# Optimization experiments

Measured on AMD Instinct MI355X. Metric: run time of the kernel, lower is better.

## Reference

```python
import jax, jax.numpy as jnp
import numpy as np

STRIDE = 1
PAD = 1
K = 3  # kernel size


def setup_inputs() -> dict:
    key = jax.random.key(0)
    k1, k2, k3, k4 = jax.random.split(key, 4)
    B, C, H, W, O = 4, 256, 64, 64, 256
    x = jax.random.normal(k1, (B, C, H, W), jnp.float32)
    offset = jax.random.normal(k2, (B, 2 * K * K, H, W), jnp.float32)
    mask = jax.random.uniform(k3, (B, K * K, H, W), jnp.float32)
    # kaiming-ish scale for the conv weight
    weight = jax.random.normal(k4, (O, C, K, K), jnp.float32) / np.float32(np.sqrt(C * K * K))
    return {"x": x, "offset": offset, "mask": mask, "weight": weight}


def _deform_conv2d(x, offset, mask, weight, stride=STRIDE, pad=PAD):
    """Modulated deformable conv v2 (torchvision deform_conv2d semantics)."""
    B, C, H, W = x.shape
    O, _, Kh, Kw = weight.shape
    KK = Kh * Kw
    Ho = (H + 2 * pad - Kh) // stride + 1
    Wo = (W + 2 * pad - Kw) // stride + 1

    # offset layout: [B, 2*KK, Ho, Wo], pairs are (dy, dx) per kernel tap
    off = offset.reshape(B, KK, 2, Ho, Wo)
    dy, dx = off[:, :, 0], off[:, :, 1]  # [B, KK, Ho, Wo]

    ki = (jnp.arange(KK) // Kw).astype(x.dtype)  # kernel row per tap
    kj = (jnp.arange(KK) % Kw).astype(x.dtype)   # kernel col per tap
    base_y = (jnp.arange(Ho) * stride - pad).astype(x.dtype)
    base_x = (jnp.arange(Wo) * stride - pad).astype(x.dtype)

    # sampling positions [B, KK, Ho, Wo]
    py = base_y[None, None, :, None] + ki[None, :, None, None] + dy
    px = base_x[None, None, None, :] + kj[None, :, None, None] + dx

    y0 = jnp.floor(py)
    x0 = jnp.floor(px)
    wy = py - y0  # fractional weights
    wx = px - x0
    y0i = y0.astype(jnp.int32)
    x0i = x0.astype(jnp.int32)

    x_bhwc = jnp.transpose(x, (0, 2, 3, 1))  # [B, H, W, C] for gathers
    b_idx = jnp.arange(B)[:, None, None, None]

    def gather(yi, xi):
        # zero outside the image (zero-padding bilinear sampling)
        valid = (yi >= 0) & (yi < H) & (xi >= 0) & (xi < W)
        v = x_bhwc[b_idx, jnp.clip(yi, 0, H - 1), jnp.clip(xi, 0, W - 1)]  # [B,KK,Ho,Wo,C]
        return v * valid[..., None].astype(x.dtype)

    one = jnp.asarray(1, x.dtype)
    sampled = (gather(y0i, x0i) * ((one - wy) * (one - wx))[..., None]
               + gather(y0i, x0i + 1) * ((one - wy) * wx)[..., None]
               + gather(y0i + 1, x0i) * (wy * (one - wx))[..., None]
               + gather(y0i + 1, x0i + 1) * (wy * wx)[..., None])

    sampled = sampled * mask.reshape(B, KK, Ho, Wo)[..., None]  # modulation

    # weighted accumulation == implicit GEMM over (c, kk)
    return jnp.einsum('bkhwc,ock->bohw', sampled, weight.reshape(O, C, KK))


def reference(x, offset, mask, weight):
    return _deform_conv2d(x, offset, mask, weight)
```

## Files before the change

kernel.cpp:

```cpp
#include <hip/hip_runtime.h>
#include <hip/hip_bf16.h>

#define CN 256
#define HN 64
#define WN 64
#define ON 256
#define KKN 9
#define HWN 4096
#define KDIM 2304
#define KC 288

using frag_ab = __attribute__((ext_vector_type(8))) short;
using frag_cd = __attribute__((ext_vector_type(4))) float;
using short4v = __attribute__((ext_vector_type(4))) short;
using int4v   = __attribute__((ext_vector_type(4))) int;
using float4v = __attribute__((ext_vector_type(4))) float;
using float2v = __attribute__((ext_vector_type(2))) float;
using uint2v  = __attribute__((ext_vector_type(2))) unsigned;

static __device__ inline short f2bf(float f) {
    union { float f; unsigned u; } v; v.f = f;
    unsigned r = v.u + 0x7fffu + ((v.u >> 16) & 1u);
    return (short)(r >> 16);
}

__global__ __launch_bounds__(256) void prep_kernel(const float* __restrict__ x,
                                                   const float* __restrict__ wsrc,
                                                   const float* __restrict__ offs,
                                                   const float* __restrict__ maskp,
                                                   short* __restrict__ xb16,
                                                   short* __restrict__ wtb,
                                                   int* __restrict__ descg) {
    int bidx = blockIdx.x;
    int tid  = threadIdx.x;
    if (bidx < 1024) {
        __shared__ float tile[64][65];
        int b   = bidx >> 8;
        int rem = bidx & 255;
        int c0  = (rem >> 6) * 64;
        int p0  = (rem & 63) * 64;
        int tp = tid & 63, tc = tid >> 6;
        for (int i = 0; i < 16; ++i) {
            int c = tc + i * 4;
            tile[c][tp] = x[(b * CN + c0 + c) * HWN + p0 + tp];
        }
        __syncthreads();
        int tcc = tid & 63, tpp = tid >> 6;
        for (int i = 0; i < 16; ++i) {
            int p = tpp + i * 4;
            xb16[(b * HWN + p0 + p) * CN + c0 + tcc] = f2bf(tile[tcc][p]);
        }
    } else if (bidx < 1312) {
        int chunk = (bidx - 1024) * 256 + tid;
        int ob  = chunk / (KC * 64);
        int rem = chunk - ob * (KC * 64);
        int kc  = rem >> 6;
        int row = rem & 63;
        int o   = ob * 64 + row;
        int kk  = kc >> 5;
        int oct = kc & 31;
        frag_ab v;
        #pragma unroll
        for (int e = 0; e < 8; ++e)
            v[e] = f2bf(wsrc[(o * CN + oct * 8 + e) * 9 + kk]);
        *(frag_ab*)&wtb[(size_t)chunk * 8] = v;
    } else {
        int u  = (bidx - 1312) * 256 + tid;
        int kk = u >> 14;
        int m  = u & 16383;
        int b  = m >> 12;
        int p  = m & 4095;
        int h  = p >> 6;
        int w  = p & 63;
        int ki = kk / 3, kj = kk - ki * 3;
        float dy = offs[(b * 18 + 2 * kk) * HWN + p];
        float dx = offs[(b * 18 + 2 * kk + 1) * HWN + p];
        float mv = maskp[(b * 9 + kk) * HWN + p];
        float py = (float)(h - 1 + ki) + dy;
        float px = (float)(w - 1 + kj) + dx;
        float y0f = floorf(py), x0f = floorf(px);
        float wy = py - y0f, wx = px - x0f;
        int y0 = (int)y0f, x0 = (int)x0f;
        int4v cb; float4v cw;
        #pragma unroll
        for (int cy = 0; cy < 2; ++cy)
            #pragma unroll
            for (int cx = 0; cx < 2; ++cx) {
                int yy = y0 + cy, xx = x0 + cx;
                bool valid = (yy >= 0 && yy < HN && xx >= 0 && xx < WN);
                int yc = min(max(yy, 0), HN - 1);
                int xc = min(max(xx, 0), WN - 1);
                cb[cy * 2 + cx] = ((b * HN + yc) * WN + xc) * CN;
                float wgt = (cy ? wy : 1.f - wy) * (cx ? wx : 1.f - wx) * mv;
                cw[cy * 2 + cx] = valid ? wgt : 0.f;
            }
        int* dd = descg + (size_t)u * 8;
        *(int4v*)dd       = cb;
        *(float4v*)(dd + 4) = cw;
    }
}

__global__ __launch_bounds__(256, 2) void fused_kernel(const short* __restrict__ xb16,
                                                       const short* __restrict__ wtb,
                                                       const int* __restrict__ descg,
                                                       float* __restrict__ out) {
    __shared__ struct {
        union {
            short Ab[2][8448];
            float outb[32 * 257];
        } mix;
        int desc[2304];
    } sm;
    int tid  = threadIdx.x;
    int m0   = blockIdx.x * 32;
    int b    = m0 >> 12;
    int h    = (m0 >> 6) & 63;
    int w0   = m0 & 63;
    int wv   = __builtin_amdgcn_readfirstlane(tid >> 6);
    int lane = tid & 63;
    int q    = lane >> 4, r = lane & 15;
    int wbase = 33 * (lane >> 1) * 8 + (lane & 1) * 4;
    int lane4 = lane * 4;
    int wv8   = wv * 8;

    #pragma unroll
    for (int kk = 0; kk < KKN; ++kk)
        sm.desc[kk * 256 + tid] = descg[((size_t)kk * 16384 + m0) * 8 + tid];
    __syncthreads();

    frag_cd acc[2][4];
    #pragma unroll
    for (int i = 0; i < 2; ++i)
        #pragma unroll
        for (int j = 0; j < 4; ++j)
            acc[i][j] = (frag_cd){0.f, 0.f, 0.f, 0.f};

    short4v stg[8][4];
    float4v cwc[8];

    auto prefetch = [&](int kk1) {
        #pragma unroll
        for (int i = 0; i < 8; ++i) {
            int dbase = (kk1 * 32 + wv8 + i) * 8;
            int4v cb = *(const int4v*)&sm.desc[dbase];
            cwc[i]   = *(const float4v*)&sm.desc[dbase + 4];
            #pragma unroll
            for (int c = 0; c < 4; ++c)
                stg[i][c] = *(const short4v*)&xb16[cb[c] + lane4];
        }
    };

    prefetch(0);

    for (int kk = 0; kk < KKN; ++kk) {
        short* dst = sm.mix.Ab[kk & 1];
        #pragma unroll
        for (int i = 0; i < 8; ++i) {
            float4v cw = cwc[i];
            short4v res;
            #pragma unroll
            for (int g = 0; g < 2; ++g) {
                float2v a = (float2v){0.f, 0.f};
                #pragma unroll
                for (int c = 0; c < 4; ++c) {
                    uint2v uv = __builtin_bit_cast(uint2v, stg[i][c]);
                    unsigned uu = uv[g];
                    float2v f;
                    f.x = __builtin_bit_cast(float, uu << 16);
                    f.y = __builtin_bit_cast(float, uu & 0xffff0000u);
                    a += f * cw[c];
                }
                __hip_bfloat162 p2 = __float22bfloat162_rn(make_float2(a.x, a.y));
                res[2 * g]     = *(short*)&p2.x;
                res[2 * g + 1] = *(short*)&p2.y;
            }
            *(short4v*)&dst[wbase + (wv8 + i) * 8] = res;
        }
        if (kk < 8) prefetch(kk + 1);
        __syncthreads();
        #pragma unroll
        for (int ks = 0; ks < 8; ++ks) {
            frag_ab af[2], bf[4];
            #pragma unroll
            for (int i = 0; i < 2; ++i)
                af[i] = *(const frag_ab*)
                    &dst[(33 * (ks * 4 + q) + i * 16 + r) * 8];
            #pragma unroll
            for (int j = 0; j < 4; ++j)
                bf[j] = *(const frag_ab*)
                    &wtb[(((size_t)wv * KC + kk * 32 + ks * 4 + q) * 64
                          + j * 16 + r) * 8];
            __builtin_amdgcn_s_setprio(1);
            #pragma unroll
            for (int i = 0; i < 2; ++i)
                #pragma unroll
                for (int j = 0; j < 4; ++j)
                    acc[i][j] = __builtin_amdgcn_mfma_f32_16x16x32_bf16(
                        af[i], bf[j], acc[i][j], 0, 0, 0);
            __builtin_amdgcn_s_setprio(0);
        }
    }
    __syncthreads();

    #pragma unroll
    for (int i = 0; i < 2; ++i)
        #pragma unroll
        for (int j = 0; j < 4; ++j) {
            int ml = i * 16 + q * 4;
            int ol = wv * 64 + j * 16 + r;
            sm.mix.outb[(ml + 0) * 257 + ol] = acc[i][j][0];
            sm.mix.outb[(ml + 1) * 257 + ol] = acc[i][j][1];
            sm.mix.outb[(ml + 2) * 257 + ol] = acc[i][j][2];
            sm.mix.outb[(ml + 3) * 257 + ol] = acc[i][j][3];
        }
    __syncthreads();
    {
        int ww = tid & 31;
        int og = tid >> 5;
        #pragma unroll
        for (int oo = 0; oo < 32; ++oo) {
            int o = oo * 8 + og;
            out[(((size_t)b * ON + o) * HN + h) * WN + w0 + ww] =
                sm.mix.outb[ww * 257 + o];
        }
    }
}

extern "C" void kernel_launch(void* const* d_in, const int* in_sizes, int n_in,
                              void* d_out, int out_size, void* d_ws, size_t ws_size,
                              hipStream_t stream) {
    const float* x      = (const float*)d_in[0];
    const float* offset = (const float*)d_in[1];
    const float* mask   = (const float*)d_in[2];
    const float* weight = (const float*)d_in[3];
    float* out = (float*)d_out;

    short* xb16  = (short*)d_ws;
    short* wtb   = (short*)((char*)d_ws + 8388608);
    int*   descg = (int*)((char*)d_ws + 9568256);

    hipLaunchKernelGGL(prep_kernel,  dim3(1888), dim3(256), 0, stream,
                       x, weight, offset, mask, xb16, wtb, descg);
    hipLaunchKernelGGL(fused_kernel, dim3(512),  dim3(256), 0, stream,
                       xb16, wtb, descg, out);
}
```

Measured before the change: 125.7 us.

## Compute sampling descriptors inside fused kernel and split work across 8 waves

Drops the descriptor-building stage from the prep kernel and computes the bilinear corner indices and weights directly into shared memory at the start of the fused kernel. This avoids the global write and read-back of the descriptor buffer. The fused kernel also moves to 512 threads (8 waves), and each wave now gathers 4 rows instead of 8 and computes a 32-column output slice instead of 64. That lowers register pressure per wave and should allow more waves resident, at the cost of more waves contending for the same shared-memory tile.

After: 121.3 us. 3.5% less time.

```diff
diff --git a/kernel.cpp b/kernel.cpp
--- a/kernel.cpp
+++ b/kernel.cpp
@@ -26,11 +26,8 @@
 
 __global__ __launch_bounds__(256) void prep_kernel(const float* __restrict__ x,
                                                    const float* __restrict__ wsrc,
-                                                   const float* __restrict__ offs,
-                                                   const float* __restrict__ maskp,
                                                    short* __restrict__ xb16,
-                                                   short* __restrict__ wtb,
-                                                   int* __restrict__ descg) {
+                                                   short* __restrict__ wtb) {
     int bidx = blockIdx.x;
     int tid  = threadIdx.x;
     if (bidx < 1024) {
@@ -50,7 +47,7 @@
             int p = tpp + i * 4;
             xb16[(b * HWN + p0 + p) * CN + c0 + tcc] = f2bf(tile[tcc][p]);
         }
-    } else if (bidx < 1312) {
+    } else {
         int chunk = (bidx - 1024) * 256 + tid;
         int ob  = chunk / (KC * 64);
         int rem = chunk - ob * (KC * 64);
@@ -64,45 +61,13 @@
         for (int e = 0; e < 8; ++e)
             v[e] = f2bf(wsrc[(o * CN + oct * 8 + e) * 9 + kk]);
         *(frag_ab*)&wtb[(size_t)chunk * 8] = v;
-    } else {
-        int u  = (bidx - 1312) * 256 + tid;
-        int kk = u >> 14;
-        int m  = u & 16383;
-        int b  = m >> 12;
-        int p  = m & 4095;
-        int h  = p >> 6;
-        int w  = p & 63;
-        int ki = kk / 3, kj = kk - ki * 3;
-        float dy = offs[(b * 18 + 2 * kk) * HWN + p];
-        float dx = offs[(b * 18 + 2 * kk + 1) * HWN + p];
-        float mv = maskp[(b * 9 + kk) * HWN + p];
-        float py = (float)(h - 1 + ki) + dy;
-        float px = (float)(w - 1 + kj) + dx;
-        float y0f = floorf(py), x0f = floorf(px);
-        float wy = py - y0f, wx = px - x0f;
-        int y0 = (int)y0f, x0 = (int)x0f;
-        int4v cb; float4v cw;
-        #pragma unroll
-        for (int cy = 0; cy < 2; ++cy)
-            #pragma unroll
-            for (int cx = 0; cx < 2; ++cx) {
-                int yy = y0 + cy, xx = x0 + cx;
-                bool valid = (yy >= 0 && yy < HN && xx >= 0 && xx < WN);
-                int yc = min(max(yy, 0), HN - 1);
-                int xc = min(max(xx, 0), WN - 1);
-                cb[cy * 2 + cx] = ((b * HN + yc) * WN + xc) * CN;
-                float wgt = (cy ? wy : 1.f - wy) * (cx ? wx : 1.f - wx) * mv;
-                cw[cy * 2 + cx] = valid ? wgt : 0.f;
-            }
-        int* dd = descg + (size_t)u * 8;
-        *(int4v*)dd       = cb;
-        *(float4v*)(dd + 4) = cw;
-    }
-}
-
-__global__ __launch_bounds__(256, 2) void fused_kernel(const short* __restrict__ xb16,
+    }
+}
+
+__global__ __launch_bounds__(512, 4) void fused_kernel(const short* __restrict__ xb16,
                                                        const short* __restrict__ wtb,
-                                                       const int* __restrict__ descg,
+                                                       const float* __restrict__ offs,
+                                                       const float* __restrict__ maskp,
                                                        float* __restrict__ out) {
     __shared__ struct {
         union {
@@ -121,27 +86,55 @@
     int q    = lane >> 4, r = lane & 15;
     int wbase = 33 * (lane >> 1) * 8 + (lane & 1) * 4;
     int lane4 = lane * 4;
-    int wv8   = wv * 8;
-
-    #pragma unroll
-    for (int kk = 0; kk < KKN; ++kk)
-        sm.desc[kk * 256 + tid] = descg[((size_t)kk * 16384 + m0) * 8 + tid];
+    int wv4   = wv * 4;
+
+    if (tid < 288) {
+        int kk = tid >> 5;
+        int m  = tid & 31;
+        int wc = w0 + m;
+        int p  = h * 64 + wc;
+        int ki = kk / 3, kj = kk - ki * 3;
+        float dy = offs[(b * 18 + 2 * kk) * HWN + p];
+        float dx = offs[(b * 18 + 2 * kk + 1) * HWN + p];
+        float mv = maskp[(b * 9 + kk) * HWN + p];
+        float py = (float)(h - 1 + ki) + dy;
+        float px = (float)(wc - 1 + kj) + dx;
+        float y0f = floorf(py), x0f = floorf(px);
+        float wy = py - y0f, wx = px - x0f;
+        int y0 = (int)y0f, x0 = (int)x0f;
+        int4v cb; float4v cw;
+        #pragma unroll
+        for (int cy = 0; cy < 2; ++cy)
+            #pragma unroll
+            for (int cx = 0; cx < 2; ++cx) {
+                int yy = y0 + cy, xx = x0 + cx;
+                bool valid = (yy >= 0 && yy < HN && xx >= 0 && xx < WN);
+                int yc = min(max(yy, 0), HN - 1);
+                int xc = min(max(xx, 0), WN - 1);
+                cb[cy * 2 + cx] = ((b * HN + yc) * WN + xc) * CN;
+                float wgt = (cy ? wy : 1.f - wy) * (cx ? wx : 1.f - wx) * mv;
+                cw[cy * 2 + cx] = valid ? wgt : 0.f;
+            }
+        int* dd = &sm.desc[tid * 8];
+        *(int4v*)dd       = cb;
+        *(float4v*)(dd + 4) = cw;
+    }
     __syncthreads();
 
-    frag_cd acc[2][4];
+    frag_cd acc[2][2];
     #pragma unroll
     for (int i = 0; i < 2; ++i)
         #pragma unroll
-        for (int j = 0; j < 4; ++j)
+        for (int j = 0; j < 2; ++j)
             acc[i][j] = (frag_cd){0.f, 0.f, 0.f, 0.f};
 
-    short4v stg[8][4];
-    float4v cwc[8];
+    short4v stg[4][4];
+    float4v cwc[4];
 
     auto prefetch = [&](int kk1) {
         #pragma unroll
-        for (int i = 0; i < 8; ++i) {
-            int dbase = (kk1 * 32 + wv8 + i) * 8;
+        for (int i = 0; i < 4; ++i) {
+            int dbase = (kk1 * 32 + wv4 + i) * 8;
             int4v cb = *(const int4v*)&sm.desc[dbase];
             cwc[i]   = *(const float4v*)&sm.desc[dbase + 4];
             #pragma unroll
@@ -152,10 +145,12 @@
 
     prefetch(0);
 
+    int jb = (wv & 1) * 2;
+    int ob = wv >> 1;
     for (int kk = 0; kk < KKN; ++kk) {
         short* dst = sm.mix.Ab[kk & 1];
         #pragma unroll
-        for (int i = 0; i < 8; ++i) {
+        for (int i = 0; i < 4; ++i) {
             float4v cw = cwc[i];
             short4v res;
             #pragma unroll
@@ -174,27 +169,27 @@
                 res[2 * g]     = *(short*)&p2.x;
                 res[2 * g + 1] = *(short*)&p2.y;
             }
-            *(short4v*)&dst[wbase + (wv8 + i) * 8] = res;
+            *(short4v*)&dst[wbase + (wv4 + i) * 8] = res;
         }
         if (kk < 8) prefetch(kk + 1);
         __syncthreads();
         #pragma unroll
         for (int ks = 0; ks < 8; ++ks) {
-            frag_ab af[2], bf[4];
+            frag_ab af[2], bf[2];
             #pragma unroll
             for (int i = 0; i < 2; ++i)
                 af[i] = *(const frag_ab*)
                     &dst[(33 * (ks * 4 + q) + i * 16 + r) * 8];
             #pragma unroll
-            for (int j = 0; j < 4; ++j)
+            for (int j = 0; j < 2; ++j)
                 bf[j] = *(const frag_ab*)
-                    &wtb[(((size_t)wv * KC + kk * 32 + ks * 4 + q) * 64
-                          + j * 16 + r) * 8];
+                    &wtb[(((size_t)ob * KC + kk * 32 + ks * 4 + q) * 64
+                          + (jb + j) * 16 + r) * 8];
             __builtin_amdgcn_s_setprio(1);
             #pragma unroll
             for (int i = 0; i < 2; ++i)
                 #pragma unroll
-                for (int j = 0; j < 4; ++j)
+                for (int j = 0; j < 2; ++j)
                     acc[i][j] = __builtin_amdgcn_mfma_f32_16x16x32_bf16(
                         af[i], bf[j], acc[i][j], 0, 0, 0);
             __builtin_amdgcn_s_setprio(0);
@@ -205,9 +200,9 @@
     #pragma unroll
     for (int i = 0; i < 2; ++i)
         #pragma unroll
-        for (int j = 0; j < 4; ++j) {
+        for (int j = 0; j < 2; ++j) {
             int ml = i * 16 + q * 4;
-            int ol = wv * 64 + j * 16 + r;
+            int ol = wv * 32 + j * 16 + r;
             sm.mix.outb[(ml + 0) * 257 + ol] = acc[i][j][0];
             sm.mix.outb[(ml + 1) * 257 + ol] = acc[i][j][1];
             sm.mix.outb[(ml + 2) * 257 + ol] = acc[i][j][2];
@@ -218,8 +213,8 @@
         int ww = tid & 31;
         int og = tid >> 5;
         #pragma unroll
-        for (int oo = 0; oo < 32; ++oo) {
-            int o = oo * 8 + og;
+        for (int oo = 0; oo < 16; ++oo) {
+            int o = oo * 16 + og;
             out[(((size_t)b * ON + o) * HN + h) * WN + w0 + ww] =
                 sm.mix.outb[ww * 257 + o];
         }
@@ -235,12 +230,11 @@
     const float* weight = (const float*)d_in[3];
     float* out = (float*)d_out;
 
-    short* xb16  = (short*)d_ws;
-    short* wtb   = (short*)((char*)d_ws + 8388608);
-    int*   descg = (int*)((char*)d_ws + 9568256);
-
-    hipLaunchKernelGGL(prep_kernel,  dim3(1888), dim3(256), 0, stream,
-                       x, weight, offset, mask, xb16, wtb, descg);
-    hipLaunchKernelGGL(fused_kernel, dim3(512),  dim3(256), 0, stream,
-                       xb16, wtb, descg, out);
-}
+    short* xb16 = (short*)d_ws;
+    short* wtb  = (short*)((char*)d_ws + 8388608);
+
+    hipLaunchKernelGGL(prep_kernel,  dim3(1312), dim3(256), 0, stream,
+                       x, weight, xb16, wtb);
+    hipLaunchKernelGGL(fused_kernel, dim3(512),  dim3(512), 0, stream,
+                       xb16, wtb, offset, mask, out);
+}
```
